# Kernel optimization log

Measured on AMD Instinct MI355X. Metric: run time of the kernel, lower is better.

The kernel has to match this reference:

```python
import jax, jax.numpy as jnp
import numpy as np

TOP_K = 4
NUM_EXPERTS = 128
HIDDEN_DIM = 2880


def setup_inputs() -> dict:
    key = jax.random.key(0)
    k1, k2, k3 = jax.random.split(key, 3)
    hidden_states = jax.random.normal(k1, (4, 4096, HIDDEN_DIM), dtype=jnp.float32)
    weight = jax.random.normal(k2, (NUM_EXPERTS, HIDDEN_DIM), dtype=jnp.float32) * 0.02
    bias = jax.random.normal(k3, (NUM_EXPERTS,), dtype=jnp.float32) * 0.02
    return {"hidden_states": hidden_states, "weight": weight, "bias": bias}


def reference(hidden_states, weight, bias):
    # flatten tokens: [T, H]
    h = hidden_states.reshape(-1, HIDDEN_DIM)
    # router logits: [T, E]
    router_logits = jnp.einsum("th,eh->te", h, weight) + bias
    # top-k over experts
    router_top_value, router_indices = jax.lax.top_k(router_logits, TOP_K)  # [T, K]
    # softmax over the k selected logits only
    router_top_value = jax.nn.softmax(router_top_value, axis=-1)
    # scatter softmaxed weights back into dense [T, E] score matrix
    T = router_logits.shape[0]
    rows = jnp.arange(T)[:, None]  # [T, 1] broadcast against [T, K]
    router_scores = jnp.zeros_like(router_logits).at[rows, router_indices].set(router_top_value)
    # histogram of expert selections
    expert_select_count = jnp.zeros((NUM_EXPERTS,), dtype=jnp.int32).at[router_indices.reshape(-1)].add(
        jnp.ones((T * TOP_K,), dtype=jnp.int32)
    )
    return router_scores, router_indices, expert_select_count
```

## Files before the change

kernel.cpp:

```cpp
#include <hip/hip_runtime.h>
#include <math.h>

#define HID 2880
#define NE  128
#define BK  32
#define TOKB 64
#define NCHG 30
#define PSTR 129

typedef _Float16 half8v __attribute__((ext_vector_type(8)));
typedef float    f32x4v __attribute__((ext_vector_type(4)));

__global__ __launch_bounds__(256)
void prep_w(const float* __restrict__ W, _Float16* __restrict__ whi,
            _Float16* __restrict__ wlo)
{
    const int e = blockIdx.x;
    for (int j = 0; j < 12; ++j) {
        const int k = j * 256 + threadIdx.x;
        if (k >= HID) break;
        const float v = W[(size_t)e * HID + k];
        const _Float16 h = (_Float16)v;
        const _Float16 l = (_Float16)(v - (float)h);
        const size_t idx = (size_t)(k >> 5) * 4096 + e * 32 + (k & 31);
        whi[idx] = h;
        wlo[idx] = l;
    }
}

#define GLOAD(dst, ptr) \
    asm volatile("global_load_dwordx4 %0, %1, off" : "=v"(dst) : "v"(ptr))
#define GLOAD_O1024(dst, ptr) \
    asm volatile("global_load_dwordx4 %0, %1, off offset:1024" : "=v"(dst) : "v"(ptr))

__global__ __launch_bounds__(768, 3)
void fused_router(const float* __restrict__ A, const _Float16* __restrict__ whi,
                  const _Float16* __restrict__ wlo, const float* __restrict__ bias,
                  float* __restrict__ scores, float* __restrict__ idxOut,
                  float* __restrict__ counts)
{
    __shared__ __align__(16) char smem[147456];
    __shared__ float sval[TOKB][4];
    __shared__ int   sidx[TOKB][4];
    __shared__ int   hist[NE];

#define SWZ(tok) ((((tok) >> 1) & 3) << 4)

    const int tid  = threadIdx.x;
    const int lane = tid & 63;
    const int wv   = __builtin_amdgcn_readfirstlane(tid >> 6);
    const int ks   = wv >> 2;
    const int wq   = wv & 3;
    const int lg   = lane >> 4;
    const int lr   = lane & 15;
    const int tokBase = blockIdx.x * TOKB;
    const int hbeg = ks * NCHG;

    const _Float16* wHp0 = whi + (size_t)((wq * 32 + lr) * 32 + lg * 8);
    const _Float16* wLp0 = wlo + (size_t)((wq * 32 + lr) * 32 + lg * 8);

    const int gid   = tid & 255;
    const int ptok  = gid >> 2;
    const int ppart = gid & 3;
    const float* aSrc = A + (size_t)(tokBase + ptok) * HID + ppart * 8;
    const int aWr = ptok * 64 + ((ppart * 16) ^ SWZ(ptok));

    int aRd[4];
#pragma unroll
    for (int n = 0; n < 4; ++n) {
        const int tok = n * 16 + lr;
        aRd[n] = tok * 64 + ((lg * 16) ^ SWZ(tok));
    }

#define WISSUE(SET, ch) do {                                                   \
    const _Float16* hp_ = wHp0 + (size_t)(ch) * 4096;                          \
    const _Float16* lp_ = wLp0 + (size_t)(ch) * 4096;                          \
    GLOAD(SET[0], hp_);                                                        \
    GLOAD(SET[1], lp_);                                                        \
    GLOAD_O1024(SET[2], hp_);                                                  \
    GLOAD_O1024(SET[3], lp_);                                                  \
} while (0)

#define CONVA1(AX, AY, SLOT) do {                                              \
    const _Float16 h0=(_Float16)AX.x, h1=(_Float16)AX.y,                       \
                   h2=(_Float16)AX.z, h3=(_Float16)AX.w;                       \
    const _Float16 h4=(_Float16)AY.x, h5=(_Float16)AY.y,                       \
                   h6=(_Float16)AY.z, h7=(_Float16)AY.w;                       \
    const half8v hh = {h0,h1,h2,h3,h4,h5,h6,h7};                               \
    const half8v ll = {(_Float16)(AX.x-(float)h0),(_Float16)(AX.y-(float)h1),  \
                       (_Float16)(AX.z-(float)h2),(_Float16)(AX.w-(float)h3),  \
                       (_Float16)(AY.x-(float)h4),(_Float16)(AY.y-(float)h5),  \
                       (_Float16)(AY.z-(float)h6),(_Float16)(AY.w-(float)h7)}; \
    char* wb_ = smem + ks * 49152 + (SLOT) * 8192 + aWr;                       \
    *reinterpret_cast<half8v*>(wb_)        = hh;                               \
    *reinterpret_cast<half8v*>(wb_ + 4096) = ll;                               \
} while (0)

#define CCHUNK(SLOT, SET) do {                                                 \
    const char* b0_ = smem + ks * 49152 + (SLOT) * 8192;                       \
    _Pragma("unroll")                                                          \
    for (int n = 0; n < 4; ++n) {                                              \
        const half8v ah = *reinterpret_cast<const half8v*>(b0_ + aRd[n]);      \
        const half8v al = *reinterpret_cast<const half8v*>(b0_ + 4096 + aRd[n]);\
        _Pragma("unroll")                                                      \
        for (int m = 0; m < 2; ++m) {                                          \
            acc[m][n] = __builtin_amdgcn_mfma_f32_16x16x32_f16(                \
                SET[m * 2 + 0], ah, acc[m][n], 0, 0, 0);                       \
            acc[m][n] = __builtin_amdgcn_mfma_f32_16x16x32_f16(                \
                SET[m * 2 + 1], ah, acc[m][n], 0, 0, 0);                       \
            acc[m][n] = __builtin_amdgcn_mfma_f32_16x16x32_f16(                \
                SET[m * 2 + 0], al, acc[m][n], 0, 0, 0);                       \
        }                                                                      \
    }                                                                          \
} while (0)

#define VMC(n) do {                                                            \
    asm volatile("s_waitcnt vmcnt(" #n ")" ::: "memory");                      \
    __builtin_amdgcn_sched_barrier(0);                                         \
} while (0)

    f32x4v acc[2][4];
#pragma unroll
    for (int m = 0; m < 2; ++m)
#pragma unroll
        for (int n = 0; n < 4; ++n) acc[m][n] = (f32x4v)0.f;

    half8v wS0[4], wS1[4], wS2[4];
    float4 aR0, aR1, aR2, aR3, aR4, aR5;

#define ASTAGE(B_) do {                                                        \
    const float* p_ = aSrc + (size_t)(hbeg + (B_)) * BK;                       \
    GLOAD(aR0, p_);      GLOAD(aR1, p_ + 4);                                   \
    GLOAD(aR2, p_ + 32); GLOAD(aR3, p_ + 36);                                  \
    GLOAD(aR4, p_ + 64); GLOAD(aR5, p_ + 68);                                  \
} while (0)

#define EPOCH(E, CS, PS, STAGE, LAST) do {                                     \
    const int b_ = 3 * (E);                                                    \
    WISSUE(wS1, hbeg + b_ + 1);                                                \
    WISSUE(wS2, hbeg + b_ + 2);                                                \
    if (STAGE) ASTAGE(b_ + 3);                                                 \
    __builtin_amdgcn_sched_barrier(0);                                         \
    CCHUNK((CS) + 0, wS0);                                                     \
    __builtin_amdgcn_sched_barrier(0);                                         \
    if (!(LAST)) { WISSUE(wS0, hbeg + b_ + 3); }                               \
    __builtin_amdgcn_sched_barrier(0);                                         \
    if (LAST) VMC(4); else VMC(14);                                            \
    CCHUNK((CS) + 1, wS1);                                                     \
    __builtin_amdgcn_sched_barrier(0);                                         \
    if (LAST) VMC(0); else VMC(10);                                            \
    CCHUNK((CS) + 2, wS2);                                                     \
    if (STAGE) {                                                               \
        VMC(0);                                                                \
        CONVA1(aR0, aR1, (PS) + 0);                                            \
        CONVA1(aR2, aR3, (PS) + 1);                                            \
        CONVA1(aR4, aR5, (PS) + 2);                                            \
        asm volatile("s_waitcnt lgkmcnt(0)" ::: "memory");                     \
        __builtin_amdgcn_sched_barrier(0);                                     \
        __builtin_amdgcn_s_barrier();                                          \
        __builtin_amdgcn_sched_barrier(0);                                     \
    }                                                                          \
} while (0)

    ASTAGE(0);
    WISSUE(wS0, hbeg + 0);
    VMC(0);
    CONVA1(aR0, aR1, 0);
    CONVA1(aR2, aR3, 1);
    CONVA1(aR4, aR5, 2);
    asm volatile("s_waitcnt lgkmcnt(0)" ::: "memory");
    __builtin_amdgcn_sched_barrier(0);
    __builtin_amdgcn_s_barrier();
    __builtin_amdgcn_sched_barrier(0);

#pragma unroll 1
    for (int e = 0; e < 8; e += 2) {
        EPOCH(e,     0, 3, 1, 0);
        EPOCH(e + 1, 3, 0, 1, 0);
    }
    EPOCH(8, 0, 3, 1, 0);
    EPOCH(9, 3, 0, 0, 1);

    __syncthreads();

    float* P1   = (float*)(smem);
    float* P2   = (float*)(smem + 33024);
    float* cval = (float*)(smem + 66048);
    int*   cidx = (int*)(smem + 74496);

    if (tid < NE) hist[tid] = 0;

    if (ks == 1 || ks == 2) {
        float* P = (ks == 1) ? P1 : P2;
#pragma unroll
        for (int m = 0; m < 2; ++m)
#pragma unroll
            for (int n = 0; n < 4; ++n)
#pragma unroll
                for (int r = 0; r < 4; ++r) {
                    const int e = wq * 32 + m * 16 + lg * 4 + r;
                    const int t = n * 16 + lr;
                    P[t * PSTR + e] = acc[m][n][r];
                }
    }
    __syncthreads();

    if (ks == 0) {
#pragma unroll
        for (int m = 0; m < 2; ++m)
#pragma unroll
            for (int n = 0; n < 4; ++n)
#pragma unroll
                for (int r = 0; r < 4; ++r) {
                    const int e = wq * 32 + m * 16 + lg * 4 + r;
                    const int t = n * 16 + lr;
                    const int off = t * PSTR + e;
                    P1[off] = ((acc[m][n][r] + P1[off]) + P2[off]) + bias[e];
                }
    }
    __syncthreads();

    if (tid < 512) {
        const int t = tid & 63, g = tid >> 6;
        float v0 = -1e30f, v1 = -1e30f, v2 = -1e30f, v3 = -1e30f;
        int   i0 = 0, i1 = 0, i2 = 0, i3 = 0;
        const int e0 = g * 16;
#pragma unroll 4
        for (int i = 0; i < 16; ++i) {
            const int e = e0 + i;
            const float v = P1[t * PSTR + e];
            if (v > v3) {
                if (v > v2) {
                    v3 = v2; i3 = i2;
                    if (v > v1) {
                        v2 = v1; i2 = i1;
                        if (v > v0) { v1 = v0; i1 = i0; v0 = v; i0 = e; }
                        else        { v1 = v;  i1 = e; }
                    } else { v2 = v; i2 = e; }
                } else { v3 = v; i3 = e; }
            }
        }
        cval[t * 33 + g * 4 + 0] = v0; cidx[t * 33 + g * 4 + 0] = i0;
        cval[t * 33 + g * 4 + 1] = v1; cidx[t * 33 + g * 4 + 1] = i1;
        cval[t * 33 + g * 4 + 2] = v2; cidx[t * 33 + g * 4 + 2] = i2;
        cval[t * 33 + g * 4 + 3] = v3; cidx[t * 33 + g * 4 + 3] = i3;
    }
    __syncthreads();

    if (tid < TOKB) {
        const int t = tid;
        float m0 = -1e30f, m1 = -1e30f, m2 = -1e30f, m3 = -1e30f;
        int   j0 = 0, j1 = 0, j2 = 0, j3 = 0;
#pragma unroll
        for (int q = 0; q < 32; ++q) {
            const float v = cval[t * 33 + q];
            const int   e = cidx[t * 33 + q];
            if (v > m3) {
                if (v > m2) {
                    m3 = m2; j3 = j2;
                    if (v > m1) {
                        m2 = m1; j2 = j1;
                        if (v > m0) { m1 = m0; j1 = j0; m0 = v; j0 = e; }
                        else        { m1 = v;  j1 = e; }
                    } else { m2 = v; j2 = e; }
                } else { m3 = v; j3 = e; }
            }
        }
        const float x1 = expf(m1 - m0), x2 = expf(m2 - m0), x3 = expf(m3 - m0);
        const float inv = 1.f / (1.f + x1 + x2 + x3);
        sval[t][0] = inv;      sidx[t][0] = j0;
        sval[t][1] = x1 * inv; sidx[t][1] = j1;
        sval[t][2] = x2 * inv; sidx[t][2] = j2;
        sval[t][3] = x3 * inv; sidx[t][3] = j3;
        atomicAdd(&hist[j0], 1); atomicAdd(&hist[j1], 1);
        atomicAdd(&hist[j2], 1); atomicAdd(&hist[j3], 1);
    }
    __syncthreads();

    const size_t sBase = (size_t)blockIdx.x * TOKB * NE;
#pragma unroll 4
    for (int it = 0; it < 11; ++it) {
        const int flat = it * 768 + tid;
        if (flat < TOKB * NE) {
            const int t = flat >> 7, e = flat & 127;
            float val = 0.f;
            val = (e == sidx[t][0]) ? sval[t][0] : val;
            val = (e == sidx[t][1]) ? sval[t][1] : val;
            val = (e == sidx[t][2]) ? sval[t][2] : val;
            val = (e == sidx[t][3]) ? sval[t][3] : val;
            scores[sBase + flat] = val;
        }
    }
    if (tid < TOKB * 4)
        idxOut[(size_t)blockIdx.x * TOKB * 4 + tid] =
            (float)sidx[tid >> 2][tid & 3];
    if (tid < NE) {
        const int c = hist[tid];
        if (c) atomicAdd(&counts[tid], (float)c);
    }
#undef SWZ
#undef WISSUE
#undef CONVA1
#undef CCHUNK
#undef VMC
#undef ASTAGE
#undef EPOCH
}

extern "C" void kernel_launch(void* const* d_in, const int* in_sizes, int n_in,
                              void* d_out, int out_size, void* d_ws, size_t ws_size,
                              hipStream_t stream) {
    const float* A = (const float*)d_in[0];
    const float* W = (const float*)d_in[1];
    const float* B = (const float*)d_in[2];
    const int T = in_sizes[0] / HID;

    float* out = (float*)d_out;
    float* scores = out;
    float* idxOut = out + (size_t)T * NE;
    float* counts = idxOut + (size_t)T * 4;

    _Float16* whi = (_Float16*)d_ws;
    _Float16* wlo = whi + (size_t)NE * HID;

    hipMemsetAsync(counts, 0, NE * sizeof(float), stream);

    hipLaunchKernelGGL(prep_w, dim3(NE), dim3(256), 0, stream, W, whi, wlo);
    hipLaunchKernelGGL(fused_router, dim3(T / TOKB), dim3(768), 0, stream,
                       A, whi, wlo, B, scores, idxOut, counts);
}
```

Baseline: 66.61 us.

## Load activations straight into registers, dropping LDS staging and barriers

The A tile is no longer staged through shared memory with a swizzled layout and per-epoch block barriers. Each wave now loads its activation fragments from global memory directly in MFMA operand layout, splits them into fp16 hi/lo in registers, and runs a simple two-deep register double buffer with weights. This removes LDS write/read traffic and the intra-loop barriers, and shrinks the shared allocation. In exchange, the four waves of each K-split group now load and convert the same activation data redundantly, and register pressure rises, which risks spills or lost latency hiding.

```diff
diff --git a/kernel.cpp b/kernel.cpp
--- a/kernel.cpp
+++ b/kernel.cpp
@@ -30,6 +30,8 @@
 
 #define GLOAD(dst, ptr) \
     asm volatile("global_load_dwordx4 %0, %1, off" : "=v"(dst) : "v"(ptr))
+#define GLOAD_O16(dst, ptr) \
+    asm volatile("global_load_dwordx4 %0, %1, off offset:16" : "=v"(dst) : "v"(ptr))
 #define GLOAD_O1024(dst, ptr) \
     asm volatile("global_load_dwordx4 %0, %1, off offset:1024" : "=v"(dst) : "v"(ptr))
 
@@ -39,12 +41,10 @@
                   float* __restrict__ scores, float* __restrict__ idxOut,
                   float* __restrict__ counts)
 {
-    __shared__ __align__(16) char smem[147456];
+    __shared__ __align__(16) char smem[82944];
     __shared__ float sval[TOKB][4];
     __shared__ int   sidx[TOKB][4];
     __shared__ int   hist[NE];
-
-#define SWZ(tok) ((((tok) >> 1) & 3) << 4)
 
     const int tid  = threadIdx.x;
     const int lane = tid & 63;
@@ -56,132 +56,85 @@
     const int tokBase = blockIdx.x * TOKB;
     const int hbeg = ks * NCHG;
 
-    const _Float16* wHp0 = whi + (size_t)((wq * 32 + lr) * 32 + lg * 8);
-    const _Float16* wLp0 = wlo + (size_t)((wq * 32 + lr) * 32 + lg * 8);
-
-    const int gid   = tid & 255;
-    const int ptok  = gid >> 2;
-    const int ppart = gid & 3;
-    const float* aSrc = A + (size_t)(tokBase + ptok) * HID + ppart * 8;
-    const int aWr = ptok * 64 + ((ppart * 16) ^ SWZ(ptok));
-
-    int aRd[4];
-#pragma unroll
-    for (int n = 0; n < 4; ++n) {
-        const int tok = n * 16 + lr;
-        aRd[n] = tok * 64 + ((lg * 16) ^ SWZ(tok));
-    }
-
-#define WISSUE(SET, ch) do {                                                   \
-    const _Float16* hp_ = wHp0 + (size_t)(ch) * 4096;                          \
-    const _Float16* lp_ = wLp0 + (size_t)(ch) * 4096;                          \
-    GLOAD(SET[0], hp_);                                                        \
-    GLOAD(SET[1], lp_);                                                        \
-    GLOAD_O1024(SET[2], hp_);                                                  \
-    GLOAD_O1024(SET[3], lp_);                                                  \
-} while (0)
-
-#define CONVA1(AX, AY, SLOT) do {                                              \
-    const _Float16 h0=(_Float16)AX.x, h1=(_Float16)AX.y,                       \
-                   h2=(_Float16)AX.z, h3=(_Float16)AX.w;                       \
-    const _Float16 h4=(_Float16)AY.x, h5=(_Float16)AY.y,                       \
-                   h6=(_Float16)AY.z, h7=(_Float16)AY.w;                       \
-    const half8v hh = {h0,h1,h2,h3,h4,h5,h6,h7};                               \
-    const half8v ll = {(_Float16)(AX.x-(float)h0),(_Float16)(AX.y-(float)h1),  \
-                       (_Float16)(AX.z-(float)h2),(_Float16)(AX.w-(float)h3),  \
-                       (_Float16)(AY.x-(float)h4),(_Float16)(AY.y-(float)h5),  \
-                       (_Float16)(AY.z-(float)h6),(_Float16)(AY.w-(float)h7)}; \
-    char* wb_ = smem + ks * 49152 + (SLOT) * 8192 + aWr;                       \
-    *reinterpret_cast<half8v*>(wb_)        = hh;                               \
-    *reinterpret_cast<half8v*>(wb_ + 4096) = ll;                               \
-} while (0)
-
-#define CCHUNK(SLOT, SET) do {                                                 \
-    const char* b0_ = smem + ks * 49152 + (SLOT) * 8192;                       \
+    const _Float16* wHp = whi + (size_t)((wq * 32 + lr) * 32 + lg * 8)
+                        + (size_t)hbeg * 4096;
+    const _Float16* wLp = wlo + (size_t)((wq * 32 + lr) * 32 + lg * 8)
+                        + (size_t)hbeg * 4096;
+
+    const float* aP[4];
+#pragma unroll
+    for (int n = 0; n < 4; ++n)
+        aP[n] = A + (size_t)(tokBase + n * 16 + lr) * HID + ks * 960 + lg * 8;
+
+#define AISSUE(BUF) do {                                                       \
     _Pragma("unroll")                                                          \
     for (int n = 0; n < 4; ++n) {                                              \
-        const half8v ah = *reinterpret_cast<const half8v*>(b0_ + aRd[n]);      \
-        const half8v al = *reinterpret_cast<const half8v*>(b0_ + 4096 + aRd[n]);\
+        GLOAD(BUF[2 * n],     aP[n]);                                          \
+        GLOAD_O16(BUF[2 * n + 1], aP[n]);                                      \
+        aP[n] += BK;                                                           \
+    }                                                                          \
+} while (0)
+
+#define WISSUE(WS) do {                                                        \
+    GLOAD(WS[0], wHp);                                                         \
+    GLOAD(WS[1], wLp);                                                         \
+    GLOAD_O1024(WS[2], wHp);                                                   \
+    GLOAD_O1024(WS[3], wLp);                                                   \
+    wHp += 4096;                                                               \
+    wLp += 4096;                                                               \
+} while (0)
+
+#define VMC(n) do {                                                            \
+    asm volatile("s_waitcnt vmcnt(" #n ")" ::: "memory");                      \
+    __builtin_amdgcn_sched_barrier(0);                                         \
+} while (0)
+
+    f32x4v acc[2][4];
+#pragma unroll
+    for (int m = 0; m < 2; ++m)
+#pragma unroll
+        for (int n = 0; n < 4; ++n) acc[m][n] = (f32x4v)0.f;
+
+    float4 a0[8], a1[8];
+    half8v w0[4], w1[4];
+
+#define CHUNK(ABUF, WBUF, DOISSUE, VMN) do {                                   \
+    VMC(VMN);                                                                  \
+    _Pragma("unroll")                                                          \
+    for (int n = 0; n < 4; ++n) {                                              \
+        const float4 u = ABUF[2 * n], v = ABUF[2 * n + 1];                     \
+        const _Float16 h0=(_Float16)u.x, h1=(_Float16)u.y,                     \
+                       h2=(_Float16)u.z, h3=(_Float16)u.w;                     \
+        const _Float16 h4=(_Float16)v.x, h5=(_Float16)v.y,                     \
+                       h6=(_Float16)v.z, h7=(_Float16)v.w;                     \
+        const half8v ah = {h0,h1,h2,h3,h4,h5,h6,h7};                           \
+        const half8v al = {(_Float16)(u.x-(float)h0),(_Float16)(u.y-(float)h1),\
+                           (_Float16)(u.z-(float)h2),(_Float16)(u.w-(float)h3),\
+                           (_Float16)(v.x-(float)h4),(_Float16)(v.y-(float)h5),\
+                           (_Float16)(v.z-(float)h6),(_Float16)(v.w-(float)h7)};\
         _Pragma("unroll")                                                      \
         for (int m = 0; m < 2; ++m) {                                          \
             acc[m][n] = __builtin_amdgcn_mfma_f32_16x16x32_f16(                \
-                SET[m * 2 + 0], ah, acc[m][n], 0, 0, 0);                       \
+                WBUF[m * 2 + 0], ah, acc[m][n], 0, 0, 0);                      \
             acc[m][n] = __builtin_amdgcn_mfma_f32_16x16x32_f16(                \
-                SET[m * 2 + 1], ah, acc[m][n], 0, 0, 0);                       \
+                WBUF[m * 2 + 1], ah, acc[m][n], 0, 0, 0);                      \
             acc[m][n] = __builtin_amdgcn_mfma_f32_16x16x32_f16(                \
-                SET[m * 2 + 0], al, acc[m][n], 0, 0, 0);                       \
+                WBUF[m * 2 + 0], al, acc[m][n], 0, 0, 0);                      \
         }                                                                      \
     }                                                                          \
-} while (0)
-
-#define VMC(n) do {                                                            \
-    asm volatile("s_waitcnt vmcnt(" #n ")" ::: "memory");                      \
-    __builtin_amdgcn_sched_barrier(0);                                         \
-} while (0)
-
-    f32x4v acc[2][4];
-#pragma unroll
-    for (int m = 0; m < 2; ++m)
-#pragma unroll
-        for (int n = 0; n < 4; ++n) acc[m][n] = (f32x4v)0.f;
-
-    half8v wS0[4], wS1[4], wS2[4];
-    float4 aR0, aR1, aR2, aR3, aR4, aR5;
-
-#define ASTAGE(B_) do {                                                        \
-    const float* p_ = aSrc + (size_t)(hbeg + (B_)) * BK;                       \
-    GLOAD(aR0, p_);      GLOAD(aR1, p_ + 4);                                   \
-    GLOAD(aR2, p_ + 32); GLOAD(aR3, p_ + 36);                                  \
-    GLOAD(aR4, p_ + 64); GLOAD(aR5, p_ + 68);                                  \
-} while (0)
-
-#define EPOCH(E, CS, PS, STAGE, LAST) do {                                     \
-    const int b_ = 3 * (E);                                                    \
-    WISSUE(wS1, hbeg + b_ + 1);                                                \
-    WISSUE(wS2, hbeg + b_ + 2);                                                \
-    if (STAGE) ASTAGE(b_ + 3);                                                 \
-    __builtin_amdgcn_sched_barrier(0);                                         \
-    CCHUNK((CS) + 0, wS0);                                                     \
-    __builtin_amdgcn_sched_barrier(0);                                         \
-    if (!(LAST)) { WISSUE(wS0, hbeg + b_ + 3); }                               \
-    __builtin_amdgcn_sched_barrier(0);                                         \
-    if (LAST) VMC(4); else VMC(14);                                            \
-    CCHUNK((CS) + 1, wS1);                                                     \
-    __builtin_amdgcn_sched_barrier(0);                                         \
-    if (LAST) VMC(0); else VMC(10);                                            \
-    CCHUNK((CS) + 2, wS2);                                                     \
-    if (STAGE) {                                                               \
-        VMC(0);                                                                \
-        CONVA1(aR0, aR1, (PS) + 0);                                            \
-        CONVA1(aR2, aR3, (PS) + 1);                                            \
-        CONVA1(aR4, aR5, (PS) + 2);                                            \
-        asm volatile("s_waitcnt lgkmcnt(0)" ::: "memory");                     \
-        __builtin_amdgcn_sched_barrier(0);                                     \
-        __builtin_amdgcn_s_barrier();                                          \
-        __builtin_amdgcn_sched_barrier(0);                                     \
-    }                                                                          \
-} while (0)
-
-    ASTAGE(0);
-    WISSUE(wS0, hbeg + 0);
-    VMC(0);
-    CONVA1(aR0, aR1, 0);
-    CONVA1(aR2, aR3, 1);
-    CONVA1(aR4, aR5, 2);
-    asm volatile("s_waitcnt lgkmcnt(0)" ::: "memory");
-    __builtin_amdgcn_sched_barrier(0);
-    __builtin_amdgcn_s_barrier();
-    __builtin_amdgcn_sched_barrier(0);
+    if (DOISSUE) { AISSUE(ABUF); WISSUE(WBUF); }                               \
+} while (0)
+
+    AISSUE(a0); WISSUE(w0);
+    AISSUE(a1); WISSUE(w1);
 
 #pragma unroll 1
-    for (int e = 0; e < 8; e += 2) {
-        EPOCH(e,     0, 3, 1, 0);
-        EPOCH(e + 1, 3, 0, 1, 0);
-    }
-    EPOCH(8, 0, 3, 1, 0);
-    EPOCH(9, 3, 0, 0, 1);
-
-    __syncthreads();
+    for (int c2 = 0; c2 < 28; c2 += 2) {
+        CHUNK(a0, w0, 1, 12);
+        CHUNK(a1, w1, 1, 12);
+    }
+    CHUNK(a0, w0, 0, 12);
+    CHUNK(a1, w1, 0, 0);
 
     float* P1   = (float*)(smem);
     float* P2   = (float*)(smem + 33024);
@@ -298,13 +251,10 @@
         const int c = hist[tid];
         if (c) atomicAdd(&counts[tid], (float)c);
     }
-#undef SWZ
+#undef AISSUE
 #undef WISSUE
-#undef CONVA1
-#undef CCHUNK
 #undef VMC
-#undef ASTAGE
-#undef EPOCH
+#undef CHUNK
 }
 
 extern "C" void kernel_launch(void* const* d_in, const int* in_sizes, int n_in,
```

New measurement: 127.1 us. +90.8%, slower.

## Restructure GEMM main loop into barrier-synchronized cells with setprio MFMA phases

Applied to the files above, without the earlier changes.

Splits each chunk's LDS fragment reads from the MFMA block and rebuilds the main loop as three cells per group. Each cell waits on global loads, reads LDS fragments, hits a workgroup barrier, then runs 24 MFMAs at raised wave priority before issuing the next weight prefetch. All three weight sets are prefetched up front. The intent is to keep waves in lockstep, with MFMA phases of one wave overlapping memory phases of others, and to prefetch deeper. It adds two barriers per chunk, which may cost sync overhead, and the vmcnt counts must stay correct or the results are wrong.

```diff
diff --git a/kernel.cpp b/kernel.cpp
--- a/kernel.cpp
+++ b/kernel.cpp
@@ -96,20 +96,26 @@
     *reinterpret_cast<half8v*>(wb_ + 4096) = ll;                               \
 } while (0)
 
-#define CCHUNK(SLOT, SET) do {                                                 \
+#define DSREAD(SLOT) do {                                                      \
     const char* b0_ = smem + ks * 49152 + (SLOT) * 8192;                       \
     _Pragma("unroll")                                                          \
     for (int n = 0; n < 4; ++n) {                                              \
-        const half8v ah = *reinterpret_cast<const half8v*>(b0_ + aRd[n]);      \
-        const half8v al = *reinterpret_cast<const half8v*>(b0_ + 4096 + aRd[n]);\
+        fh[n] = *reinterpret_cast<const half8v*>(b0_ + aRd[n]);                \
+        fl[n] = *reinterpret_cast<const half8v*>(b0_ + 4096 + aRd[n]);         \
+    }                                                                          \
+} while (0)
+
+#define MFMA24(SET) do {                                                       \
+    _Pragma("unroll")                                                          \
+    for (int n = 0; n < 4; ++n) {                                              \
         _Pragma("unroll")                                                      \
         for (int m = 0; m < 2; ++m) {                                          \
             acc[m][n] = __builtin_amdgcn_mfma_f32_16x16x32_f16(                \
-                SET[m * 2 + 0], ah, acc[m][n], 0, 0, 0);                       \
+                SET[m * 2 + 0], fh[n], acc[m][n], 0, 0, 0);                    \
             acc[m][n] = __builtin_amdgcn_mfma_f32_16x16x32_f16(                \
-                SET[m * 2 + 1], ah, acc[m][n], 0, 0, 0);                       \
+                SET[m * 2 + 1], fh[n], acc[m][n], 0, 0, 0);                    \
             acc[m][n] = __builtin_amdgcn_mfma_f32_16x16x32_f16(                \
-                SET[m * 2 + 0], al, acc[m][n], 0, 0, 0);                       \
+                SET[m * 2 + 0], fl[n], acc[m][n], 0, 0, 0);                    \
         }                                                                      \
     }                                                                          \
 } while (0)
@@ -119,6 +125,10 @@
     __builtin_amdgcn_sched_barrier(0);                                         \
 } while (0)
 
+#define SB0   __builtin_amdgcn_sched_barrier(0)
+#define BAR   do { SB0; __builtin_amdgcn_s_barrier(); SB0; } while (0)
+#define LGKM0 do { asm volatile("s_waitcnt lgkmcnt(0)" ::: "memory"); SB0; } while (0)
+
     f32x4v acc[2][4];
 #pragma unroll
     for (int m = 0; m < 2; ++m)
@@ -126,6 +136,7 @@
         for (int n = 0; n < 4; ++n) acc[m][n] = (f32x4v)0.f;
 
     half8v wS0[4], wS1[4], wS2[4];
+    half8v fh[4], fl[4];
     float4 aR0, aR1, aR2, aR3, aR4, aR5;
 
 #define ASTAGE(B_) do {                                                        \
@@ -135,51 +146,64 @@
     GLOAD(aR4, p_ + 64); GLOAD(aR5, p_ + 68);                                  \
 } while (0)
 
-#define EPOCH(E, CS, PS, STAGE, LAST) do {                                     \
-    const int b_ = 3 * (E);                                                    \
-    WISSUE(wS1, hbeg + b_ + 1);                                                \
-    WISSUE(wS2, hbeg + b_ + 2);                                                \
-    if (STAGE) ASTAGE(b_ + 3);                                                 \
-    __builtin_amdgcn_sched_barrier(0);                                         \
-    CCHUNK((CS) + 0, wS0);                                                     \
-    __builtin_amdgcn_sched_barrier(0);                                         \
-    if (!(LAST)) { WISSUE(wS0, hbeg + b_ + 3); }                               \
-    __builtin_amdgcn_sched_barrier(0);                                         \
-    if (LAST) VMC(4); else VMC(14);                                            \
-    CCHUNK((CS) + 1, wS1);                                                     \
-    __builtin_amdgcn_sched_barrier(0);                                         \
-    if (LAST) VMC(0); else VMC(10);                                            \
-    CCHUNK((CS) + 2, wS2);                                                     \
-    if (STAGE) {                                                               \
-        VMC(0);                                                                \
-        CONVA1(aR0, aR1, (PS) + 0);                                            \
-        CONVA1(aR2, aR3, (PS) + 1);                                            \
-        CONVA1(aR4, aR5, (PS) + 2);                                            \
-        asm volatile("s_waitcnt lgkmcnt(0)" ::: "memory");                     \
-        __builtin_amdgcn_sched_barrier(0);                                     \
-        __builtin_amdgcn_s_barrier();                                          \
-        __builtin_amdgcn_sched_barrier(0);                                     \
+#define CELL0(G, VMN) do {                                                     \
+    if ((G) < 9) ASTAGE(3 * (G) + 3);                                          \
+    SB0;                                                                       \
+    VMC(VMN);                                                                  \
+    DSREAD(((G) & 1) * 3 + 0);                                                 \
+    BAR;                                                                       \
+    LGKM0;                                                                     \
+    __builtin_amdgcn_s_setprio(1); MFMA24(wS0); __builtin_amdgcn_s_setprio(0); \
+    if (3 * (G) + 3 < NCHG) WISSUE(wS0, hbeg + 3 * (G) + 3);                   \
+    BAR;                                                                       \
+} while (0)
+
+#define CELL1(G, VMN) do {                                                     \
+    VMC(VMN);                                                                  \
+    DSREAD(((G) & 1) * 3 + 1);                                                 \
+    BAR;                                                                       \
+    LGKM0;                                                                     \
+    __builtin_amdgcn_s_setprio(1); MFMA24(wS1); __builtin_amdgcn_s_setprio(0); \
+    if (3 * (G) + 4 < NCHG) WISSUE(wS1, hbeg + 3 * (G) + 4);                   \
+    BAR;                                                                       \
+} while (0)
+
+#define CELL2(G, VMN) do {                                                     \
+    VMC(VMN);                                                                  \
+    if ((G) < 9) {                                                             \
+        const int ps_ = (((G) & 1) * 3) ^ 3;          \
+        CONVA1(aR0, aR1, ps_ + 0);                                             \
+        CONVA1(aR2, aR3, ps_ + 1);                                             \
+        CONVA1(aR4, aR5, ps_ + 2);                                             \
     }                                                                          \
+    DSREAD(((G) & 1) * 3 + 2);                                                 \
+    BAR;                                                                       \
+    LGKM0;                                                                     \
+    __builtin_amdgcn_s_setprio(1); MFMA24(wS2); __builtin_amdgcn_s_setprio(0); \
+    if (3 * (G) + 5 < NCHG) WISSUE(wS2, hbeg + 3 * (G) + 5);                   \
+    BAR;                                                                       \
 } while (0)
 
     ASTAGE(0);
     WISSUE(wS0, hbeg + 0);
-    VMC(0);
+    WISSUE(wS1, hbeg + 1);
+    WISSUE(wS2, hbeg + 2);
+    VMC(12);
     CONVA1(aR0, aR1, 0);
     CONVA1(aR2, aR3, 1);
     CONVA1(aR4, aR5, 2);
-    asm volatile("s_waitcnt lgkmcnt(0)" ::: "memory");
-    __builtin_amdgcn_sched_barrier(0);
-    __builtin_amdgcn_s_barrier();
-    __builtin_amdgcn_sched_barrier(0);
+    LGKM0;
+    BAR;
 
 #pragma unroll 1
-    for (int e = 0; e < 8; e += 2) {
-        EPOCH(e,     0, 3, 1, 0);
-        EPOCH(e + 1, 3, 0, 1, 0);
-    }
-    EPOCH(8, 0, 3, 1, 0);
-    EPOCH(9, 3, 0, 0, 1);
+    for (int g = 0; g < 9; ++g) {
+        CELL0(g, 14);
+        CELL1(g, 14);
+        CELL2(g, 8);
+    }
+    CELL0(9, 8);
+    CELL1(9, 4);
+    CELL2(9, 0);
 
     __syncthreads();
 
@@ -301,10 +325,16 @@
 #undef SWZ
 #undef WISSUE
 #undef CONVA1
-#undef CCHUNK
+#undef DSREAD
+#undef MFMA24
 #undef VMC
+#undef SB0
+#undef BAR
+#undef LGKM0
 #undef ASTAGE
-#undef EPOCH
+#undef CELL0
+#undef CELL1
+#undef CELL2
 }
 
 extern "C" void kernel_launch(void* const* d_in, const int* in_sizes, int n_in,
```

Result: slower. 73.98 us (+11.1%).

## Split router GEMM into 2 K-slices x 2 token halves with 1024-thread blocks

Applied to the files above, without the earlier changes.

The work split changes from 3 K-slices of 30 chunks each with 4 waves per slice to 2 K-slices of 45 chunks each. Each slice now has 8 waves, which split the 64 tokens into two halves. Shared memory falls from 144KB to 96KB, the partial-sum reduction loses one buffer, and the A staging loads switch to float4 per thread. The aim is to raise waves per block and cut LDS use, but the two token halves each reload the same W fragments, which doubles W traffic per block.

```diff
diff --git a/kernel.cpp b/kernel.cpp
--- a/kernel.cpp
+++ b/kernel.cpp
@@ -5,9 +5,10 @@
 #define NE  128
 #define BK  32
 #define TOKB 64
-#define NCHG 30
+#define NCHG 45
 #define PSTR 129
 
+typedef _Float16 half4v __attribute__((ext_vector_type(4)));
 typedef _Float16 half8v __attribute__((ext_vector_type(8)));
 typedef float    f32x4v __attribute__((ext_vector_type(4)));
 
@@ -33,13 +34,13 @@
 #define GLOAD_O1024(dst, ptr) \
     asm volatile("global_load_dwordx4 %0, %1, off offset:1024" : "=v"(dst) : "v"(ptr))
 
-__global__ __launch_bounds__(768, 3)
+__global__ __launch_bounds__(1024, 4)
 void fused_router(const float* __restrict__ A, const _Float16* __restrict__ whi,
                   const _Float16* __restrict__ wlo, const float* __restrict__ bias,
                   float* __restrict__ scores, float* __restrict__ idxOut,
                   float* __restrict__ counts)
 {
-    __shared__ __align__(16) char smem[147456];
+    __shared__ __align__(16) char smem[98304];
     __shared__ float sval[TOKB][4];
     __shared__ int   sidx[TOKB][4];
     __shared__ int   hist[NE];
@@ -49,8 +50,10 @@
     const int tid  = threadIdx.x;
     const int lane = tid & 63;
     const int wv   = __builtin_amdgcn_readfirstlane(tid >> 6);
-    const int ks   = wv >> 2;
-    const int wq   = wv & 3;
+    const int ks   = wv >> 3;
+    const int sub  = wv & 7;
+    const int wq   = sub & 3;
+    const int th   = sub >> 2;
     const int lg   = lane >> 4;
     const int lr   = lane & 15;
     const int tokBase = blockIdx.x * TOKB;
@@ -59,16 +62,16 @@
     const _Float16* wHp0 = whi + (size_t)((wq * 32 + lr) * 32 + lg * 8);
     const _Float16* wLp0 = wlo + (size_t)((wq * 32 + lr) * 32 + lg * 8);
 
-    const int gid   = tid & 255;
-    const int ptok  = gid >> 2;
-    const int ppart = gid & 3;
-    const float* aSrc = A + (size_t)(tokBase + ptok) * HID + ppart * 8;
-    const int aWr = ptok * 64 + ((ppart * 16) ^ SWZ(ptok));
-
-    int aRd[4];
-#pragma unroll
-    for (int n = 0; n < 4; ++n) {
-        const int tok = n * 16 + lr;
+    const int gid  = tid & 511;
+    const int ptok = gid >> 3;
+    const int part = gid & 7;
+    const float* aSrc = A + (size_t)(tokBase + ptok) * HID + ks * 1440 + part * 4;
+    const int aWr = ptok * 64 + ((part * 8) ^ SWZ(ptok));
+
+    int aRd[2];
+#pragma unroll
+    for (int n = 0; n < 2; ++n) {
+        const int tok = th * 32 + n * 16 + lr;
         aRd[n] = tok * 64 + ((lg * 16) ^ SWZ(tok));
     }
 
@@ -81,25 +84,21 @@
     GLOAD_O1024(SET[3], lp_);                                                  \
 } while (0)
 
-#define CONVA1(AX, AY, SLOT) do {                                              \
+#define CONVA1(AX, SLOT) do {                                                  \
     const _Float16 h0=(_Float16)AX.x, h1=(_Float16)AX.y,                       \
                    h2=(_Float16)AX.z, h3=(_Float16)AX.w;                       \
-    const _Float16 h4=(_Float16)AY.x, h5=(_Float16)AY.y,                       \
-                   h6=(_Float16)AY.z, h7=(_Float16)AY.w;                       \
-    const half8v hh = {h0,h1,h2,h3,h4,h5,h6,h7};                               \
-    const half8v ll = {(_Float16)(AX.x-(float)h0),(_Float16)(AX.y-(float)h1),  \
-                       (_Float16)(AX.z-(float)h2),(_Float16)(AX.w-(float)h3),  \
-                       (_Float16)(AY.x-(float)h4),(_Float16)(AY.y-(float)h5),  \
-                       (_Float16)(AY.z-(float)h6),(_Float16)(AY.w-(float)h7)}; \
+    const half4v hh = {h0,h1,h2,h3};                                           \
+    const half4v ll = {(_Float16)(AX.x-(float)h0),(_Float16)(AX.y-(float)h1),  \
+                       (_Float16)(AX.z-(float)h2),(_Float16)(AX.w-(float)h3)}; \
     char* wb_ = smem + ks * 49152 + (SLOT) * 8192 + aWr;                       \
-    *reinterpret_cast<half8v*>(wb_)        = hh;                               \
-    *reinterpret_cast<half8v*>(wb_ + 4096) = ll;                               \
+    *reinterpret_cast<half4v*>(wb_)        = hh;                               \
+    *reinterpret_cast<half4v*>(wb_ + 4096) = ll;                               \
 } while (0)
 
 #define CCHUNK(SLOT, SET) do {                                                 \
     const char* b0_ = smem + ks * 49152 + (SLOT) * 8192;                       \
     _Pragma("unroll")                                                          \
-    for (int n = 0; n < 4; ++n) {                                              \
+    for (int n = 0; n < 2; ++n) {                                              \
         const half8v ah = *reinterpret_cast<const half8v*>(b0_ + aRd[n]);      \
         const half8v al = *reinterpret_cast<const half8v*>(b0_ + 4096 + aRd[n]);\
         _Pragma("unroll")                                                      \
@@ -119,20 +118,24 @@
     __builtin_amdgcn_sched_barrier(0);                                         \
 } while (0)
 
-    f32x4v acc[2][4];
+#define SB0   __builtin_amdgcn_sched_barrier(0)
+#define LGKM0 do { asm volatile("s_waitcnt lgkmcnt(0)" ::: "memory"); SB0; } while (0)
+#define BAR   do { SB0; __builtin_amdgcn_s_barrier(); SB0; } while (0)
+
+    f32x4v acc[2][2];
 #pragma unroll
     for (int m = 0; m < 2; ++m)
 #pragma unroll
-        for (int n = 0; n < 4; ++n) acc[m][n] = (f32x4v)0.f;
+        for (int n = 0; n < 2; ++n) acc[m][n] = (f32x4v)0.f;
 
     half8v wS0[4], wS1[4], wS2[4];
-    float4 aR0, aR1, aR2, aR3, aR4, aR5;
+    float4 aR0, aR1, aR2;
 
 #define ASTAGE(B_) do {                                                        \
-    const float* p_ = aSrc + (size_t)(hbeg + (B_)) * BK;                       \
-    GLOAD(aR0, p_);      GLOAD(aR1, p_ + 4);                                   \
-    GLOAD(aR2, p_ + 32); GLOAD(aR3, p_ + 36);                                  \
-    GLOAD(aR4, p_ + 64); GLOAD(aR5, p_ + 68);                                  \
+    const float* p_ = aSrc + (size_t)(B_) * BK;                                \
+    GLOAD(aR0, p_);                                                            \
+    GLOAD(aR1, p_ + BK);                                                       \
+    GLOAD(aR2, p_ + 2 * BK);                                                   \
 } while (0)
 
 #define EPOCH(E, CS, PS, STAGE, LAST) do {                                     \
@@ -140,67 +143,60 @@
     WISSUE(wS1, hbeg + b_ + 1);                                                \
     WISSUE(wS2, hbeg + b_ + 2);                                                \
     if (STAGE) ASTAGE(b_ + 3);                                                 \
-    __builtin_amdgcn_sched_barrier(0);                                         \
+    SB0;                                                                       \
     CCHUNK((CS) + 0, wS0);                                                     \
-    __builtin_amdgcn_sched_barrier(0);                                         \
+    SB0;                                                                       \
     if (!(LAST)) { WISSUE(wS0, hbeg + b_ + 3); }                               \
-    __builtin_amdgcn_sched_barrier(0);                                         \
-    if (LAST) VMC(4); else VMC(14);                                            \
+    SB0;                                                                       \
+    if (LAST) VMC(4); else VMC(11);                                            \
     CCHUNK((CS) + 1, wS1);                                                     \
-    __builtin_amdgcn_sched_barrier(0);                                         \
-    if (LAST) VMC(0); else VMC(10);                                            \
+    SB0;                                                                       \
+    if (LAST) VMC(0); else VMC(7);                                             \
     CCHUNK((CS) + 2, wS2);                                                     \
     if (STAGE) {                                                               \
         VMC(0);                                                                \
-        CONVA1(aR0, aR1, (PS) + 0);                                            \
-        CONVA1(aR2, aR3, (PS) + 1);                                            \
-        CONVA1(aR4, aR5, (PS) + 2);                                            \
-        asm volatile("s_waitcnt lgkmcnt(0)" ::: "memory");                     \
-        __builtin_amdgcn_sched_barrier(0);                                     \
-        __builtin_amdgcn_s_barrier();                                          \
-        __builtin_amdgcn_sched_barrier(0);                                     \
+        CONVA1(aR0, (PS) + 0);                                                 \
+        CONVA1(aR1, (PS) + 1);                                                 \
+        CONVA1(aR2, (PS) + 2);                                                 \
+        LGKM0;                                                                 \
+        BAR;                                                                   \
     }                                                                          \
 } while (0)
 
     ASTAGE(0);
     WISSUE(wS0, hbeg + 0);
     VMC(0);
-    CONVA1(aR0, aR1, 0);
-    CONVA1(aR2, aR3, 1);
-    CONVA1(aR4, aR5, 2);
-    asm volatile("s_waitcnt lgkmcnt(0)" ::: "memory");
-    __builtin_amdgcn_sched_barrier(0);
-    __builtin_amdgcn_s_barrier();
-    __builtin_amdgcn_sched_barrier(0);
+    CONVA1(aR0, 0);
+    CONVA1(aR1, 1);
+    CONVA1(aR2, 2);
+    LGKM0;
+    BAR;
 
 #pragma unroll 1
-    for (int e = 0; e < 8; e += 2) {
+    for (int e = 0; e < 14; e += 2) {
         EPOCH(e,     0, 3, 1, 0);
         EPOCH(e + 1, 3, 0, 1, 0);
     }
-    EPOCH(8, 0, 3, 1, 0);
-    EPOCH(9, 3, 0, 0, 1);
+    EPOCH(14, 0, 3, 0, 1);
 
     __syncthreads();
 
     float* P1   = (float*)(smem);
-    float* P2   = (float*)(smem + 33024);
-    float* cval = (float*)(smem + 66048);
-    int*   cidx = (int*)(smem + 74496);
+    float* cval = (float*)(smem + 33024);
+    int*   cidx = (int*)(smem + 41472);
 
     if (tid < NE) hist[tid] = 0;
 
-    if (ks == 1 || ks == 2) {
-        float* P = (ks == 1) ? P1 : P2;
+    if (ks == 1) {
 #pragma unroll
         for (int m = 0; m < 2; ++m)
 #pragma unroll
-            for (int n = 0; n < 4; ++n)
+            for (int n = 0; n < 2; ++n)
 #pragma unroll
                 for (int r = 0; r < 4; ++r) {
                     const int e = wq * 32 + m * 16 + lg * 4 + r;
-                    const int t = n * 16 + lr;
-                    P[t * PSTR + e] = acc[m][n][r];
+                    const int t = th * 32 + n * 16 + lr;
+                    P1[t * PSTR + e] = acc[m][n][r];
                 }
     }
     __syncthreads();
@@ -209,13 +205,13 @@
 #pragma unroll
         for (int m = 0; m < 2; ++m)
 #pragma unroll
-            for (int n = 0; n < 4; ++n)
+            for (int n = 0; n < 2; ++n)
 #pragma unroll
                 for (int r = 0; r < 4; ++r) {
                     const int e = wq * 32 + m * 16 + lg * 4 + r;
-                    const int t = n * 16 + lr;
+                    const int t = th * 32 + n * 16 + lr;
                     const int off = t * PSTR + e;
-                    P1[off] = ((acc[m][n][r] + P1[off]) + P2[off]) + bias[e];
+                    P1[off] = (acc[m][n][r] + P1[off]) + bias[e];
                 }
     }
     __syncthreads();
@@ -279,17 +275,15 @@
 
     const size_t sBase = (size_t)blockIdx.x * TOKB * NE;
 #pragma unroll 4
-    for (int it = 0; it < 11; ++it) {
-        const int flat = it * 768 + tid;
-        if (flat < TOKB * NE) {
-            const int t = flat >> 7, e = flat & 127;
-            float val = 0.f;
-            val = (e == sidx[t][0]) ? sval[t][0] : val;
-            val = (e == sidx[t][1]) ? sval[t][1] : val;
-            val = (e == sidx[t][2]) ? sval[t][2] : val;
-            val = (e == sidx[t][3]) ? sval[t][3] : val;
-            scores[sBase + flat] = val;
-        }
+    for (int it = 0; it < 8; ++it) {
+        const int flat = it * 1024 + tid;
+        const int t = flat >> 7, e = flat & 127;
+        float val = 0.f;
+        val = (e == sidx[t][0]) ? sval[t][0] : val;
+        val = (e == sidx[t][1]) ? sval[t][1] : val;
+        val = (e == sidx[t][2]) ? sval[t][2] : val;
+        val = (e == sidx[t][3]) ? sval[t][3] : val;
+        scores[sBase + flat] = val;
     }
     if (tid < TOKB * 4)
         idxOut[(size_t)blockIdx.x * TOKB * 4 + tid] =
@@ -303,6 +297,9 @@
 #undef CONVA1
 #undef CCHUNK
 #undef VMC
+#undef SB0
+#undef LGKM0
+#undef BAR
 #undef ASTAGE
 #undef EPOCH
 }
@@ -326,6 +323,6 @@
     hipMemsetAsync(counts, 0, NE * sizeof(float), stream);
 
     hipLaunchKernelGGL(prep_w, dim3(NE), dim3(256), 0, stream, W, whi, wlo);
-    hipLaunchKernelGGL(fused_router, dim3(T / TOKB), dim3(768), 0, stream,
+    hipLaunchKernelGGL(fused_router, dim3(T / TOKB), dim3(1024), 0, stream,
                        A, whi, wlo, B, scores, idxOut, counts);
 }
```

New measurement: 81.34 us. 1.22x slower.
